# Optimization experiments

Measured on AMD Instinct MI355X. Metric: run time of the kernel, lower is better.

## Reference

```python
import jax, jax.numpy as jnp
import numpy as np

N = 50000
H = 128          # hidden/in/out channels
F = 128          # num_filters
R = 64           # num_rbf
E = 1_600_000    # graph edges
K = 3            # discrete kernel size
RC = 5.0         # cutoff radius


def setup_inputs() -> dict:
    key = jax.random.key(0)
    ks = jax.random.split(key, 16)
    x = jax.random.normal(ks[0], (N, H), dtype=jnp.float32)
    edge_index = jax.random.randint(ks[1], (2, E), 0, N)
    edge_weight = jax.random.uniform(ks[2], (E,), dtype=jnp.float32) * RC
    edge_attr = jax.random.normal(ks[3], (E, R), dtype=jnp.float32)
    # sequential +/-1 neighbor edges (get_seq_neigh): src-dst in {+1,-1}
    i = jnp.arange(N - 1)
    src = jnp.concatenate([i + 1, i])
    dst = jnp.concatenate([i, i + 1])
    disc_edge_index = jnp.stack([src, dst])  # (2, 2*(N-1))

    def xavier(k, shape):
        fan_in, fan_out = shape[1], shape[0]
        lim = jnp.sqrt(6.0 / (fan_in + fan_out)).astype(jnp.float32)
        return jax.random.uniform(k, shape, jnp.float32, -lim, lim)

    return {
        "x": x,
        "edge_weight": edge_weight,
        "edge_attr": edge_attr,
        # filter network: Linear(R,F) -> tanh -> Linear(F,F)
        "fw1": xavier(ks[4], (F, R)), "fb1": jnp.zeros((F,), jnp.float32),
        "fw2": xavier(ks[5], (F, F)), "fb2": jnp.zeros((F,), jnp.float32),
        "lin1_w": xavier(ks[6], (F, H)),                 # no bias
        "lin2_w": xavier(ks[7], (H, F)), "lin2_b": jnp.zeros((H,), jnp.float32),
        "disc_w": xavier(ks[8], (K, F)),                 # DiscConv weight
        "lin_w": xavier(ks[9], (H, H)), "lin_b": jnp.zeros((H,), jnp.float32),
        "edge_index": edge_index,
        "disc_edge_index": disc_edge_index,
    }


def reference(x, edge_weight, edge_attr, fw1, fb1, fw2, fb2,
              lin1_w, lin2_w, lin2_b, disc_w, lin_w, lin_b,
              edge_index, disc_edge_index):
    n = x.shape[0]
    # cosine cutoff envelope
    C = 0.5 * (jnp.cos(edge_weight * (jnp.pi / RC)) + 1.0)
    C = jnp.where(edge_weight < RC, C, 0.0)
    # filter network on expanded distances
    W = jnp.tanh(edge_attr @ fw1.T + fb1) @ fw2.T + fb2
    W = W * C[:, None]                                   # (E, F)
    # lin1 (no bias)
    h = x @ lin1_w.T                                     # (N, F)
    # gather-multiply-scatter message passing
    src, dst = edge_index[0], edge_index[1]
    msg = h[src] * W                                     # (E, F)
    agg = jax.ops.segment_sum(msg, dst, num_segments=n)  # (N, F)
    # discrete sequential convolution (DiscConv)
    dsrc, ddst = disc_edge_index[0], disc_edge_index[1]
    widx = jnp.mod(dsrc - ddst, K)                       # torch weight[-1] == weight[K-1]
    dmsg = disc_w[widx] * h[dsrc]
    disc_out = jax.ops.segment_sum(dmsg, ddst, num_segments=n) + disc_w[0] * h
    h = agg + disc_out
    # lin2 -> tanh -> interaction-block lin
    h = h @ lin2_w.T + lin2_b
    h = jnp.tanh(h)
    return h @ lin_w.T + lin_b
```

## Files before the change

kernel.cpp:

```cpp
#include <hip/hip_runtime.h>
#include <math.h>

#define HD 128
#define FD 128
#define RD 64
#define TE 128
#define RC_CUT 5.0f

typedef _Float16 half8_t __attribute__((ext_vector_type(8)));
typedef float floatx4 __attribute__((ext_vector_type(4)));

__device__ __forceinline__ float fast_tanh(float x) {
    float ex = __expf(2.0f * x);
    return 1.0f - 2.0f / (ex + 1.0f);
}

__global__ __launch_bounds__(256) void lin1_kernel(const float* __restrict__ x,
                                                   const float* __restrict__ w,
                                                   float* __restrict__ h, int n)
{
    __shared__ float sx[16][HD];
    int base = blockIdx.x * 16;
    for (int i = threadIdx.x; i < 16 * HD; i += 256) {
        int r = i >> 7, c = i & 127;
        int row = base + r;
        sx[r][c] = (row < n) ? x[(size_t)row * HD + c] : 0.0f;
    }
    __syncthreads();
    int f = threadIdx.x & 127;
    int half = threadIdx.x >> 7;
    float acc[8];
#pragma unroll
    for (int r = 0; r < 8; ++r) acc[r] = 0.0f;
    const float* wrow = w + (size_t)f * HD;
    for (int k = 0; k < HD; ++k) {
        float wv = wrow[k];
#pragma unroll
        for (int r = 0; r < 8; ++r) acc[r] += sx[half * 8 + r][k] * wv;
    }
#pragma unroll
    for (int r = 0; r < 8; ++r) {
        int row = base + half * 8 + r;
        if (row < n) h[(size_t)row * FD + f] = acc[r];
    }
}

__device__ __forceinline__ half8_t lds_read8(const char* base, int row,
                                             int rowstride, int col) {
    int off = row * rowstride + ((col * 2) ^ ((row & 7) << 4));
    return *(const half8_t*)(base + off);
}

__global__ __launch_bounds__(1024, 8) void edge_kernel(
    const float* __restrict__ edge_weight,
    const float* __restrict__ edge_attr,
    const float* __restrict__ fw1, const float* __restrict__ fb1,
    const float* __restrict__ fw2, const float* __restrict__ fb2,
    const int* __restrict__ eidx,
    const float* __restrict__ h,
    float* agg, int E, int ntiles)
{
    extern __shared__ char smem[];
    char* sT  = smem;
    char* sB1 = smem + 32768;
    char* sB2 = smem + 49152;

    for (int i = threadIdx.x * 8; i < FD * RD; i += blockDim.x * 8) {
        int r = i >> 6, c = i & 63;
        const float4* g = (const float4*)(fw1 + (size_t)r * RD + c);
        float4 v0 = g[0], v1 = g[1];
        half8_t hv;
        hv[0] = (_Float16)v0.x; hv[1] = (_Float16)v0.y;
        hv[2] = (_Float16)v0.z; hv[3] = (_Float16)v0.w;
        hv[4] = (_Float16)v1.x; hv[5] = (_Float16)v1.y;
        hv[6] = (_Float16)v1.z; hv[7] = (_Float16)v1.w;
        *(half8_t*)(sB1 + r * 128 + ((c * 2) ^ ((r & 7) << 4))) = hv;
    }
    for (int i = threadIdx.x * 8; i < FD * FD; i += blockDim.x * 8) {
        int r = i >> 7, c = i & 127;
        const float4* g = (const float4*)(fw2 + (size_t)r * FD + c);
        float4 v0 = g[0], v1 = g[1];
        half8_t hv;
        hv[0] = (_Float16)v0.x; hv[1] = (_Float16)v0.y;
        hv[2] = (_Float16)v0.z; hv[3] = (_Float16)v0.w;
        hv[4] = (_Float16)v1.x; hv[5] = (_Float16)v1.y;
        hv[6] = (_Float16)v1.z; hv[7] = (_Float16)v1.w;
        *(half8_t*)(sB2 + r * 256 + ((c * 2) ^ ((r & 7) << 4))) = hv;
    }
    __syncthreads();

    const int* srcp = eidx;
    const int* dstp = eidx + E;
    int lane = threadIdx.x & 63;
    int wid  = threadIdx.x >> 6;
    int wm = wid >> 2;
    int wn = wid & 3;
    int l15 = lane & 15;
    int l4  = lane >> 4;

    for (int tile = blockIdx.x; tile < ntiles; tile += gridDim.x) {
        int e0 = tile * TE;
        for (int i = threadIdx.x * 8; i < TE * RD; i += blockDim.x * 8) {
            int r = i >> 6, c = i & 63;
            half8_t hv;
            if (e0 + r < E) {
                const float4* g = (const float4*)(edge_attr + (size_t)(e0 + r) * RD + c);
                float4 v0 = g[0], v1 = g[1];
                hv[0] = (_Float16)v0.x; hv[1] = (_Float16)v0.y;
                hv[2] = (_Float16)v0.z; hv[3] = (_Float16)v0.w;
                hv[4] = (_Float16)v1.x; hv[5] = (_Float16)v1.y;
                hv[6] = (_Float16)v1.z; hv[7] = (_Float16)v1.w;
            } else {
                for (int q = 0; q < 8; ++q) hv[q] = (_Float16)0.0f;
            }
            *(half8_t*)(sT + r * 128 + ((c * 2) ^ ((r & 7) << 4))) = hv;
        }
        __syncthreads();

        floatx4 acc[2][2];
#pragma unroll
        for (int mi = 0; mi < 2; ++mi)
#pragma unroll
            for (int ni = 0; ni < 2; ++ni)
                acc[mi][ni] = (floatx4){0.f, 0.f, 0.f, 0.f};
#pragma unroll
        for (int ks = 0; ks < 2; ++ks) {
            int k = ks * 32 + l4 * 8;
            half8_t a[2], b[2];
#pragma unroll
            for (int mi = 0; mi < 2; ++mi)
                a[mi] = lds_read8(sT, wm * 32 + mi * 16 + l15, 128, k);
#pragma unroll
            for (int ni = 0; ni < 2; ++ni)
                b[ni] = lds_read8(sB1, wn * 32 + ni * 16 + l15, 128, k);
#pragma unroll
            for (int mi = 0; mi < 2; ++mi)
#pragma unroll
                for (int ni = 0; ni < 2; ++ni)
                    acc[mi][ni] = __builtin_amdgcn_mfma_f32_16x16x32_f16(
                        a[mi], b[ni], acc[mi][ni], 0, 0, 0);
        }
        __syncthreads();

#pragma unroll
        for (int ni = 0; ni < 2; ++ni) {
            int f = wn * 32 + ni * 16 + l15;
            float bias = fb1[f];
#pragma unroll
            for (int mi = 0; mi < 2; ++mi) {
#pragma unroll
                for (int j = 0; j < 4; ++j) {
                    int e = wm * 32 + mi * 16 + l4 * 4 + j;
                    float t = fast_tanh(acc[mi][ni][j] + bias);
                    *(_Float16*)(sT + e * 256 + ((f * 2) ^ ((e & 7) << 4))) =
                        (_Float16)t;
                }
            }
        }
        __syncthreads();

        floatx4 acc2[2][2];
#pragma unroll
        for (int mi = 0; mi < 2; ++mi)
#pragma unroll
            for (int ni = 0; ni < 2; ++ni)
                acc2[mi][ni] = (floatx4){0.f, 0.f, 0.f, 0.f};
#pragma unroll
        for (int ks = 0; ks < 4; ++ks) {
            int k = ks * 32 + l4 * 8;
            half8_t a[2], b[2];
#pragma unroll
            for (int mi = 0; mi < 2; ++mi)
                a[mi] = lds_read8(sT, wm * 32 + mi * 16 + l15, 256, k);
#pragma unroll
            for (int ni = 0; ni < 2; ++ni)
                b[ni] = lds_read8(sB2, wn * 32 + ni * 16 + l15, 256, k);
#pragma unroll
            for (int mi = 0; mi < 2; ++mi)
#pragma unroll
                for (int ni = 0; ni < 2; ++ni)
                    acc2[mi][ni] = __builtin_amdgcn_mfma_f32_16x16x32_f16(
                        a[mi], b[ni], acc2[mi][ni], 0, 0, 0);
        }
        __syncthreads();

        float bias2[2];
        int gcol[2];
#pragma unroll
        for (int ni = 0; ni < 2; ++ni) {
            gcol[ni] = wn * 32 + ni * 16 + l15;
            bias2[ni] = fb2[gcol[ni]];
        }
#pragma unroll
        for (int mi = 0; mi < 2; ++mi) {
            int ge[4], s4[4], dn4[4];
            float d4[4];
#pragma unroll
            for (int j = 0; j < 4; ++j) {
                int el = wm * 32 + mi * 16 + l4 * 4 + j;
                ge[j] = e0 + el;
                int idx = (ge[j] < E) ? ge[j] : (E - 1);
                s4[j]  = srcp[idx];
                dn4[j] = dstp[idx];
                d4[j]  = edge_weight[idx];
            }
#pragma unroll
            for (int j = 0; j < 4; ++j) {
                if (ge[j] >= E) continue;
                float C = (d4[j] < RC_CUT)
                            ? 0.5f * (__cosf(d4[j] * 0.6283185307179586f) + 1.0f)
                            : 0.0f;
                const float* hrow = h + (size_t)s4[j] * FD;
                float* ar = agg + (size_t)dn4[j] * FD;
#pragma unroll
                for (int ni = 0; ni < 2; ++ni) {
                    int g = gcol[ni];
                    float wv = (acc2[mi][ni][j] + bias2[ni]) * C;
                    atomicAdd(ar + g, wv * hrow[g]);
                }
            }
        }
    }
}

__global__ __launch_bounds__(256) void final_kernel(
    const float* aggin, const float* __restrict__ h,
    const float* __restrict__ disc_w,
    const float* __restrict__ lin2_w, const float* __restrict__ lin2_b,
    const float* __restrict__ lin_w, const float* __restrict__ lin_b,
    float* out, int n)
{
    __shared__ float sg[16][FD];
    __shared__ float sm[16][FD];
    int base = blockIdx.x * 16;
    for (int i = threadIdx.x; i < 16 * FD; i += 256) {
        int r = i >> 7, c = i & 127;
        int row = base + r;
        float v = 0.0f;
        if (row < n) {
            v = aggin[(size_t)row * FD + c] + disc_w[c] * h[(size_t)row * FD + c];
            if (row + 1 < n) v += disc_w[FD + c] * h[(size_t)(row + 1) * FD + c];
            if (row >= 1)    v += disc_w[2 * FD + c] * h[(size_t)(row - 1) * FD + c];
        }
        sg[r][c] = v;
    }
    __syncthreads();
    int f = threadIdx.x & 127;
    int half = threadIdx.x >> 7;
    {
        float acc[8];
        float b = lin2_b[f];
#pragma unroll
        for (int r = 0; r < 8; ++r) acc[r] = b;
        const float* wrow = lin2_w + (size_t)f * FD;
        for (int k = 0; k < FD; ++k) {
            float wv = wrow[k];
#pragma unroll
            for (int r = 0; r < 8; ++r) acc[r] += sg[half * 8 + r][k] * wv;
        }
#pragma unroll
        for (int r = 0; r < 8; ++r) sm[half * 8 + r][f] = fast_tanh(acc[r]);
    }
    __syncthreads();
    {
        float acc[8];
        float b = lin_b[f];
#pragma unroll
        for (int r = 0; r < 8; ++r) acc[r] = b;
        const float* wrow = lin_w + (size_t)f * HD;
        for (int k = 0; k < FD; ++k) {
            float wv = wrow[k];
#pragma unroll
            for (int r = 0; r < 8; ++r) acc[r] += sm[half * 8 + r][k] * wv;
        }
#pragma unroll
        for (int r = 0; r < 8; ++r) {
            int row = base + half * 8 + r;
            if (row < n) out[(size_t)row * HD + f] = acc[r];
        }
    }
}

extern "C" void kernel_launch(void* const* d_in, const int* in_sizes, int n_in,
                              void* d_out, int out_size, void* d_ws, size_t ws_size,
                              hipStream_t stream)
{
    const float* x      = (const float*)d_in[0];
    const float* ew     = (const float*)d_in[1];
    const float* ea     = (const float*)d_in[2];
    const float* fw1    = (const float*)d_in[3];
    const float* fb1    = (const float*)d_in[4];
    const float* fw2    = (const float*)d_in[5];
    const float* fb2    = (const float*)d_in[6];
    const float* lin1_w = (const float*)d_in[7];
    const float* lin2_w = (const float*)d_in[8];
    const float* lin2_b = (const float*)d_in[9];
    const float* disc_w = (const float*)d_in[10];
    const float* lin_w  = (const float*)d_in[11];
    const float* lin_b  = (const float*)d_in[12];
    const int*   eidx   = (const int*)d_in[13];

    int n = in_sizes[0] / HD;
    int E = in_sizes[1];
    float* out = (float*)d_out;
    float* h   = (float*)d_ws;

    hipMemsetAsync(d_out, 0, (size_t)out_size * sizeof(float), stream);

    lin1_kernel<<<(n + 15) / 16, 256, 0, stream>>>(x, lin1_w, h, n);

    int ntiles = (E + TE - 1) / TE;
    size_t smem = 81920;
    hipFuncSetAttribute((const void*)edge_kernel,
                        hipFuncAttributeMaxDynamicSharedMemorySize, (int)smem);
    int nblocks = ntiles < 512 ? ntiles : 512;
    edge_kernel<<<nblocks, 1024, smem, stream>>>(ew, ea, fw1, fb1, fw2, fb2,
                                                 eidx, h, out, E, ntiles);

    final_kernel<<<(n + 15) / 16, 256, 0, stream>>>(out, h, disc_w, lin2_w, lin2_b,
                                                    lin_w, lin_b, out, n);
}
```

Baseline: 876.4 us.

## Bucket edges by destination window and accumulate messages in shared memory

Adds a counting sort of edges into 16-node destination buckets (count, scan, scatter kernels). The edge kernel then pulls buckets from a global work queue, runs the filter MLP on each bucket's edges, and accumulates messages with LDS atomics into a swizzled 16x128 shared buffer. Each bucket writes its rows to agg once, so the global float atomics go away. In exchange it adds three preprocessing passes with global atomics, a serial single-wavefront scan, and indirect gathers of edge_attr, src, dst and weight through perm, which lose coalescing.

Result: slower. 2.399 ms (+173.8%).

```diff
diff --git a/kernel.cpp b/kernel.cpp
--- a/kernel.cpp
+++ b/kernel.cpp
@@ -6,6 +6,8 @@
 #define RD 64
 #define TE 128
 #define RC_CUT 5.0f
+#define WIN 16
+#define WIN_SHIFT 4
 
 typedef _Float16 half8_t __attribute__((ext_vector_type(8)));
 typedef float floatx4 __attribute__((ext_vector_type(4)));
@@ -45,25 +47,72 @@
     }
 }
 
+__global__ __launch_bounds__(256) void count_kernel(const int* __restrict__ dstp,
+                                                    int* cnt, int E)
+{
+    for (int e = blockIdx.x * blockDim.x + threadIdx.x; e < E;
+         e += gridDim.x * blockDim.x)
+        atomicAdd(&cnt[dstp[e] >> WIN_SHIFT], 1);
+}
+
+__global__ void scan_kernel(int* cnt, int* offs, int nbk)
+{
+    int lane = threadIdx.x;
+    int carry = 0;
+    for (int base = 0; base < nbk; base += 64) {
+        int i = base + lane;
+        int v = (i < nbk) ? cnt[i] : 0;
+        int orig = v;
+#pragma unroll
+        for (int d = 1; d < 64; d <<= 1) {
+            int t = __shfl_up(v, d);
+            if (lane >= d) v += t;
+        }
+        if (i < nbk) {
+            int excl = carry + v - orig;
+            offs[i] = excl;
+            cnt[i]  = excl;
+        }
+        carry += __shfl(v, 63);
+    }
+    if (lane == 0) offs[nbk] = carry;
+}
+
+__global__ __launch_bounds__(256) void scatter_kernel(const int* __restrict__ dstp,
+                                                      int* cursor, int* perm, int E)
+{
+    for (int e = blockIdx.x * blockDim.x + threadIdx.x; e < E;
+         e += gridDim.x * blockDim.x) {
+        int p = atomicAdd(&cursor[dstp[e] >> WIN_SHIFT], 1);
+        perm[p] = e;
+    }
+}
+
 __device__ __forceinline__ half8_t lds_read8(const char* base, int row,
                                              int rowstride, int col) {
     int off = row * rowstride + ((col * 2) ^ ((row & 7) << 4));
     return *(const half8_t*)(base + off);
 }
 
-__global__ __launch_bounds__(1024, 8) void edge_kernel(
+__global__ __launch_bounds__(1024, 4) void edge_kernel(
     const float* __restrict__ edge_weight,
     const float* __restrict__ edge_attr,
     const float* __restrict__ fw1, const float* __restrict__ fb1,
     const float* __restrict__ fw2, const float* __restrict__ fb2,
     const int* __restrict__ eidx,
     const float* __restrict__ h,
-    float* agg, int E, int ntiles)
+    const int* __restrict__ perm,
+    const int* __restrict__ offs,
+    int* qctr,
+    float* __restrict__ agg,
+    int E, int n, int nbk)
 {
     extern __shared__ char smem[];
-    char* sT  = smem;
-    char* sB1 = smem + 32768;
-    char* sB2 = smem + 49152;
+    char*  sT   = smem;
+    char*  sB1  = smem + 32768;
+    char*  sB2  = smem + 49152;
+    float* sAgg = (float*)(smem + 81920);
+    __shared__ int sBkt;
 
     for (int i = threadIdx.x * 8; i < FD * RD; i += blockDim.x * 8) {
         int r = i >> 6, c = i & 63;
@@ -87,7 +136,7 @@
         hv[6] = (_Float16)v1.z; hv[7] = (_Float16)v1.w;
         *(half8_t*)(sB2 + r * 256 + ((c * 2) ^ ((r & 7) << 4))) = hv;
     }
-    __syncthreads();
+    for (int i = threadIdx.x; i < WIN * FD; i += blockDim.x) sAgg[i] = 0.0f;
 
     const int* srcp = eidx;
     const int* dstp = eidx + E;
@@ -98,128 +147,157 @@
     int l15 = lane & 15;
     int l4  = lane >> 4;
 
-    for (int tile = blockIdx.x; tile < ntiles; tile += gridDim.x) {
-        int e0 = tile * TE;
-        for (int i = threadIdx.x * 8; i < TE * RD; i += blockDim.x * 8) {
-            int r = i >> 6, c = i & 63;
-            half8_t hv;
-            if (e0 + r < E) {
-                const float4* g = (const float4*)(edge_attr + (size_t)(e0 + r) * RD + c);
-                float4 v0 = g[0], v1 = g[1];
-                hv[0] = (_Float16)v0.x; hv[1] = (_Float16)v0.y;
-                hv[2] = (_Float16)v0.z; hv[3] = (_Float16)v0.w;
-                hv[4] = (_Float16)v1.x; hv[5] = (_Float16)v1.y;
-                hv[6] = (_Float16)v1.z; hv[7] = (_Float16)v1.w;
-            } else {
-                for (int q = 0; q < 8; ++q) hv[q] = (_Float16)0.0f;
+    float bias2[2];
+    float bias1[2];
+    int gcol[2];
+#pragma unroll
+    for (int ni = 0; ni < 2; ++ni) {
+        gcol[ni]  = wn * 32 + ni * 16 + l15;
+        bias2[ni] = fb2[gcol[ni]];
+        bias1[ni] = fb1[gcol[ni]];
+    }
+
+    while (true) {
+        if (threadIdx.x == 0) sBkt = atomicAdd(qctr, 1);
+        __syncthreads();
+        int bkt = sBkt;
+        if (bkt >= nbk) break;
+        int offs0 = offs[bkt];
+        int nE    = offs[bkt + 1] - offs0;
+
+        for (int t0 = 0; t0 < nE; t0 += TE) {
+            {
+                int i = threadIdx.x * 8;
+                int r = i >> 6, c = i & 63;
+                half8_t hv;
+                int ei = t0 + r;
+                if (ei < nE) {
+                    int e = perm[offs0 + ei];
+                    const float4* g = (const float4*)(edge_attr + (size_t)e * RD + c);
+                    float4 v0 = g[0], v1 = g[1];
+                    hv[0] = (_Float16)v0.x; hv[1] = (_Float16)v0.y;
+                    hv[2] = (_Float16)v0.z; hv[3] = (_Float16)v0.w;
+                    hv[4] = (_Float16)v1.x; hv[5] = (_Float16)v1.y;
+                    hv[6] = (_Float16)v1.z; hv[7] = (_Float16)v1.w;
+                } else {
+                    for (int q = 0; q < 8; ++q) hv[q] = (_Float16)0.0f;
+                }
+                *(half8_t*)(sT + r * 128 + ((c * 2) ^ ((r & 7) << 4))) = hv;
             }
-            *(half8_t*)(sT + r * 128 + ((c * 2) ^ ((r & 7) << 4))) = hv;
-        }
-        __syncthreads();
-
-        floatx4 acc[2][2];
-#pragma unroll
-        for (int mi = 0; mi < 2; ++mi)
-#pragma unroll
-            for (int ni = 0; ni < 2; ++ni)
-                acc[mi][ni] = (floatx4){0.f, 0.f, 0.f, 0.f};
-#pragma unroll
-        for (int ks = 0; ks < 2; ++ks) {
-            int k = ks * 32 + l4 * 8;
-            half8_t a[2], b[2];
+            __syncthreads();
+
+            floatx4 acc[2][2];
 #pragma unroll
             for (int mi = 0; mi < 2; ++mi)
-                a[mi] = lds_read8(sT, wm * 32 + mi * 16 + l15, 128, k);
-#pragma unroll
-            for (int ni = 0; ni < 2; ++ni)
-                b[ni] = lds_read8(sB1, wn * 32 + ni * 16 + l15, 128, k);
-#pragma unroll
-            for (int mi = 0; mi < 2; ++mi)
 #pragma unroll
                 for (int ni = 0; ni < 2; ++ni)
-                    acc[mi][ni] = __builtin_amdgcn_mfma_f32_16x16x32_f16(
-                        a[mi], b[ni], acc[mi][ni], 0, 0, 0);
-        }
-        __syncthreads();
-
-#pragma unroll
-        for (int ni = 0; ni < 2; ++ni) {
-            int f = wn * 32 + ni * 16 + l15;
-            float bias = fb1[f];
-#pragma unroll
-            for (int mi = 0; mi < 2; ++mi) {
-#pragma unroll
-                for (int j = 0; j < 4; ++j) {
-                    int e = wm * 32 + mi * 16 + l4 * 4 + j;
-                    float t = fast_tanh(acc[mi][ni][j] + bias);
-                    *(_Float16*)(sT + e * 256 + ((f * 2) ^ ((e & 7) << 4))) =
-                        (_Float16)t;
+                    acc[mi][ni] = (floatx4){0.f, 0.f, 0.f, 0.f};
+#pragma unroll
+            for (int ks = 0; ks < 2; ++ks) {
+                int k = ks * 32 + l4 * 8;
+                half8_t a[2], b[2];
+#pragma unroll
+                for (int mi = 0; mi < 2; ++mi)
+                    a[mi] = lds_read8(sT, wm * 32 + mi * 16 + l15, 128, k);
+#pragma unroll
+                for (int ni = 0; ni < 2; ++ni)
+                    b[ni] = lds_read8(sB1, wn * 32 + ni * 16 + l15, 128, k);
+#pragma unroll
+                for (int mi = 0; mi < 2; ++mi)
+#pragma unroll
+                    for (int ni = 0; ni < 2; ++ni)
+                        acc[mi][ni] = __builtin_amdgcn_mfma_f32_16x16x32_f16(
+                            a[mi], b[ni], acc[mi][ni], 0, 0, 0);
+            }
+            __syncthreads();
+
+#pragma unroll
+            for (int ni = 0; ni < 2; ++ni) {
+                int f = gcol[ni];
+                float bias = bias1[ni];
+#pragma unroll
+                for (int mi = 0; mi < 2; ++mi) {
+#pragma unroll
+                    for (int j = 0; j < 4; ++j) {
+                        int e = wm * 32 + mi * 16 + l4 * 4 + j;
+                        float t = fast_tanh(acc[mi][ni][j] + bias);
+                        *(_Float16*)(sT + e * 256 + ((f * 2) ^ ((e & 7) << 4))) =
+                            (_Float16)t;
+                    }
                 }
             }
-        }
-        __syncthreads();
-
-        floatx4 acc2[2][2];
-#pragma unroll
-        for (int mi = 0; mi < 2; ++mi)
-#pragma unroll
-            for (int ni = 0; ni < 2; ++ni)
-                acc2[mi][ni] = (floatx4){0.f, 0.f, 0.f, 0.f};
-#pragma unroll
-        for (int ks = 0; ks < 4; ++ks) {
-            int k = ks * 32 + l4 * 8;
-            half8_t a[2], b[2];
+            __syncthreads();
+
+            floatx4 acc2[2][2];
 #pragma unroll
             for (int mi = 0; mi < 2; ++mi)
-                a[mi] = lds_read8(sT, wm * 32 + mi * 16 + l15, 256, k);
-#pragma unroll
-            for (int ni = 0; ni < 2; ++ni)
-                b[ni] = lds_read8(sB2, wn * 32 + ni * 16 + l15, 256, k);
-#pragma unroll
-            for (int mi = 0; mi < 2; ++mi)
 #pragma unroll
                 for (int ni = 0; ni < 2; ++ni)
-                    acc2[mi][ni] = __builtin_amdgcn_mfma_f32_16x16x32_f16(
-                        a[mi], b[ni], acc2[mi][ni], 0, 0, 0);
-        }
-        __syncthreads();
-
-        float bias2[2];
-        int gcol[2];
-#pragma unroll
-        for (int ni = 0; ni < 2; ++ni) {
-            gcol[ni] = wn * 32 + ni * 16 + l15;
-            bias2[ni] = fb2[gcol[ni]];
-        }
-#pragma unroll
-        for (int mi = 0; mi < 2; ++mi) {
-            int ge[4], s4[4], dn4[4];
-            float d4[4];
-#pragma unroll
-            for (int j = 0; j < 4; ++j) {
-                int el = wm * 32 + mi * 16 + l4 * 4 + j;
-                ge[j] = e0 + el;
-                int idx = (ge[j] < E) ? ge[j] : (E - 1);
-                s4[j]  = srcp[idx];
-                dn4[j] = dstp[idx];
-                d4[j]  = edge_weight[idx];
+                    acc2[mi][ni] = (floatx4){0.f, 0.f, 0.f, 0.f};
+#pragma unroll
+            for (int ks = 0; ks < 4; ++ks) {
+                int k = ks * 32 + l4 * 8;
+                half8_t a[2], b[2];
+#pragma unroll
+                for (int mi = 0; mi < 2; ++mi)
+                    a[mi] = lds_read8(sT, wm * 32 + mi * 16 + l15, 256, k);
+#pragma unroll
+                for (int ni = 0; ni < 2; ++ni)
+                    b[ni] = lds_read8(sB2, wn * 32 + ni * 16 + l15, 256, k);
+#pragma unroll
+                for (int mi = 0; mi < 2; ++mi)
+#pragma unroll
+                    for (int ni = 0; ni < 2; ++ni)
+                        acc2[mi][ni] = __builtin_amdgcn_mfma_f32_16x16x32_f16(
+                            a[mi], b[ni], acc2[mi][ni], 0, 0, 0);
             }
-#pragma unroll
-            for (int j = 0; j < 4; ++j) {
-                if (ge[j] >= E) continue;
-                float C = (d4[j] < RC_CUT)
-                            ? 0.5f * (__cosf(d4[j] * 0.6283185307179586f) + 1.0f)
-                            : 0.0f;
-                const float* hrow = h + (size_t)s4[j] * FD;
-                float* ar = agg + (size_t)dn4[j] * FD;
-#pragma unroll
-                for (int ni = 0; ni < 2; ++ni) {
-                    int g = gcol[ni];
-                    float wv = (acc2[mi][ni][j] + bias2[ni]) * C;
-                    atomicAdd(ar + g, wv * hrow[g]);
+            __syncthreads();
+
+#pragma unroll
+            for (int mi = 0; mi < 2; ++mi) {
+                int e4[4], s4[4], lr4[4], ok4[4];
+                float d4[4];
+#pragma unroll
+                for (int j = 0; j < 4; ++j) {
+                    int el = wm * 32 + mi * 16 + l4 * 4 + j;
+                    int ei = t0 + el;
+                    ok4[j] = (ei < nE);
+                    e4[j]  = perm[offs0 + (ok4[j] ? ei : 0)];
+                }
+#pragma unroll
+                for (int j = 0; j < 4; ++j) {
+                    s4[j]  = srcp[e4[j]];
+                    lr4[j] = dstp[e4[j]] - (bkt << WIN_SHIFT);
+                    d4[j]  = edge_weight[e4[j]];
+                }
+#pragma unroll
+                for (int j = 0; j < 4; ++j) {
+                    if (!ok4[j]) continue;
+                    float C = (d4[j] < RC_CUT)
+                                ? 0.5f * (__cosf(d4[j] * 0.6283185307179586f) + 1.0f)
+                                : 0.0f;
+                    const float* hrow = h + (size_t)s4[j] * FD;
+                    float* arow = sAgg + lr4[j] * FD;
+                    int rot = (lr4[j] & 7) << 2;
+#pragma unroll
+                    for (int ni = 0; ni < 2; ++ni) {
+                        int g = gcol[ni];
+                        float wv = (acc2[mi][ni][j] + bias2[ni]) * C;
+                        atomicAdd(arow + (g ^ rot), wv * hrow[g]);
+                    }
                 }
             }
         }
+        __syncthreads();
+
+        for (int idx = threadIdx.x; idx < WIN * FD; idx += blockDim.x) {
+            int r = idx >> 7, c = idx & 127;
+            int row = (bkt << WIN_SHIFT) + r;
+            int sa = r * FD + (c ^ ((r & 7) << 2));
+            if (row < n) agg[(size_t)row * FD + c] = sAgg[sa];
+            sAgg[sa] = 0.0f;
+        }
+        __syncthreads();
     }
 }
 
@@ -302,20 +380,33 @@
 
     int n = in_sizes[0] / HD;
     int E = in_sizes[1];
+    int nbk = (n + WIN - 1) / WIN;
     float* out = (float*)d_out;
-    float* h   = (float*)d_ws;
+
+    char* base = (char*)d_ws;
+    float* h    = (float*)base;
+    int*   perm = (int*)(base + (size_t)n * FD * 4);
+    int*   cnt  = (int*)(base + (size_t)n * FD * 4 + (size_t)E * 4);
+    int*   offs = cnt + nbk;
+    int*   qctr = offs + nbk + 1;
+
+    const int* dstp = eidx + E;
 
     hipMemsetAsync(d_out, 0, (size_t)out_size * sizeof(float), stream);
+    hipMemsetAsync(cnt, 0, (size_t)(2 * nbk + 2) * sizeof(int), stream);
+
+    count_kernel<<<2048, 256, 0, stream>>>(dstp, cnt, E);
+    scan_kernel<<<1, 64, 0, stream>>>(cnt, offs, nbk);
+    scatter_kernel<<<2048, 256, 0, stream>>>(dstp, cnt, perm, E);
 
     lin1_kernel<<<(n + 15) / 16, 256, 0, stream>>>(x, lin1_w, h, n);
 
-    int ntiles = (E + TE - 1) / TE;
-    size_t smem = 81920;
+    size_t smem = 90112;
     hipFuncSetAttribute((const void*)edge_kernel,
                         hipFuncAttributeMaxDynamicSharedMemorySize, (int)smem);
-    int nblocks = ntiles < 512 ? ntiles : 512;
-    edge_kernel<<<nblocks, 1024, smem, stream>>>(ew, ea, fw1, fb1, fw2, fb2,
-                                                 eidx, h, out, E, ntiles);
+    edge_kernel<<<256, 1024, smem, stream>>>(ew, ea, fw1, fb1, fw2, fb2,
+                                             eidx, h, perm, offs, qctr,
+                                             out, E, n, nbk);
 
     final_kernel<<<(n + 15) / 16, 256, 0, stream>>>(out, h, disc_w, lin2_w, lin2_b,
                                                     lin_w, lin_b, out, n);
```

## Bucket edges by destination window and aggregate in shared memory

Applied to the files above, without the earlier changes.

Adds a counting sort of edges by 16-node destination windows (count, scan and scatter kernels). The filter-network GEMM kernel now writes the per-edge fp16 filter W into the sorted position. A new aggregation kernel then gathers h, multiplies, and accumulates each window in LDS with shared-memory atomics instead of global float atomics. This removes global atomic contention, but adds a large fp16 W round trip through memory plus several preprocessing launches. The old atomic kernel remains as a fallback when the workspace is too small or n exceeds 16-bit indices.

After: 1.916 ms. 119% more time.

```diff
diff --git a/kernel.cpp b/kernel.cpp
--- a/kernel.cpp
+++ b/kernel.cpp
@@ -6,6 +6,8 @@
 #define RD 64
 #define TE 128
 #define RC_CUT 5.0f
+#define WIN 16
+#define WIN_SHIFT 4
 
 typedef _Float16 half8_t __attribute__((ext_vector_type(8)));
 typedef float floatx4 __attribute__((ext_vector_type(4)));
@@ -45,20 +47,64 @@
     }
 }
 
+__global__ __launch_bounds__(256) void count_kernel(const int* __restrict__ dstp,
+                                                    int* cnt, int E)
+{
+    for (int e = blockIdx.x * blockDim.x + threadIdx.x; e < E;
+         e += gridDim.x * blockDim.x)
+        atomicAdd(&cnt[dstp[e] >> WIN_SHIFT], 1);
+}
+
+__global__ void scan_kernel(int* cnt, int* offs, int nbk)
+{
+    int lane = threadIdx.x;
+    int carry = 0;
+    for (int base = 0; base < nbk; base += 64) {
+        int i = base + lane;
+        int v = (i < nbk) ? cnt[i] : 0;
+        int orig = v;
+#pragma unroll
+        for (int d = 1; d < 64; d <<= 1) {
+            int t = __shfl_up(v, d);
+            if (lane >= d) v += t;
+        }
+        if (i < nbk) {
+            int excl = carry + v - orig;
+            offs[i] = excl;
+            cnt[i]  = excl;
+        }
+        carry += __shfl(v, 63);
+    }
+    if (lane == 0) offs[nbk] = carry;
+}
+
+__global__ __launch_bounds__(256) void scatter_kernel(
+    const int* __restrict__ srcp, const int* __restrict__ dstp,
+    int* cursor, int* __restrict__ inv, unsigned int* __restrict__ meta, int E)
+{
+    for (int e = blockIdx.x * blockDim.x + threadIdx.x; e < E;
+         e += gridDim.x * blockDim.x) {
+        int d = dstp[e];
+        int p = atomicAdd(&cursor[d >> WIN_SHIFT], 1);
+        inv[e] = p;
+        meta[p] = (unsigned int)srcp[e] | ((unsigned int)(d & (WIN - 1)) << 16);
+    }
+}
+
 __device__ __forceinline__ half8_t lds_read8(const char* base, int row,
                                              int rowstride, int col) {
     int off = row * rowstride + ((col * 2) ^ ((row & 7) << 4));
     return *(const half8_t*)(base + off);
 }
 
-__global__ __launch_bounds__(1024, 8) void edge_kernel(
+__global__ __launch_bounds__(1024, 8) void edge_gemm_kernel(
     const float* __restrict__ edge_weight,
     const float* __restrict__ edge_attr,
     const float* __restrict__ fw1, const float* __restrict__ fb1,
     const float* __restrict__ fw2, const float* __restrict__ fb2,
-    const int* __restrict__ eidx,
-    const float* __restrict__ h,
-    float* agg, int E, int ntiles)
+    const int* __restrict__ inv,
+    _Float16* __restrict__ Wp,
+    int E, int ntiles)
 {
     extern __shared__ char smem[];
     char* sT  = smem;
@@ -89,14 +135,21 @@
     }
     __syncthreads();
 
-    const int* srcp = eidx;
-    const int* dstp = eidx + E;
     int lane = threadIdx.x & 63;
     int wid  = threadIdx.x >> 6;
     int wm = wid >> 2;
     int wn = wid & 3;
     int l15 = lane & 15;
     int l4  = lane >> 4;
+
+    float bias1[2], bias2[2];
+    int gcol[2];
+#pragma unroll
+    for (int ni = 0; ni < 2; ++ni) {
+        gcol[ni]  = wn * 32 + ni * 16 + l15;
+        bias1[ni] = fb1[gcol[ni]];
+        bias2[ni] = fb2[gcol[ni]];
+    }
 
     for (int tile = blockIdx.x; tile < ntiles; tile += gridDim.x) {
         int e0 = tile * TE;
@@ -144,6 +197,206 @@
 
 #pragma unroll
         for (int ni = 0; ni < 2; ++ni) {
+            int f = gcol[ni];
+            float bias = bias1[ni];
+#pragma unroll
+            for (int mi = 0; mi < 2; ++mi) {
+#pragma unroll
+                for (int j = 0; j < 4; ++j) {
+                    int e = wm * 32 + mi * 16 + l4 * 4 + j;
+                    float t = fast_tanh(acc[mi][ni][j] + bias);
+                    *(_Float16*)(sT + e * 256 + ((f * 2) ^ ((e & 7) << 4))) =
+                        (_Float16)t;
+                }
+            }
+        }
+        __syncthreads();
+
+        floatx4 acc2[2][2];
+#pragma unroll
+        for (int mi = 0; mi < 2; ++mi)
+#pragma unroll
+            for (int ni = 0; ni < 2; ++ni)
+                acc2[mi][ni] = (floatx4){0.f, 0.f, 0.f, 0.f};
+#pragma unroll
+        for (int ks = 0; ks < 4; ++ks) {
+            int k = ks * 32 + l4 * 8;
+            half8_t a[2], b[2];
+#pragma unroll
+            for (int mi = 0; mi < 2; ++mi)
+                a[mi] = lds_read8(sT, wm * 32 + mi * 16 + l15, 256, k);
+#pragma unroll
+            for (int ni = 0; ni < 2; ++ni)
+                b[ni] = lds_read8(sB2, wn * 32 + ni * 16 + l15, 256, k);
+#pragma unroll
+            for (int mi = 0; mi < 2; ++mi)
+#pragma unroll
+                for (int ni = 0; ni < 2; ++ni)
+                    acc2[mi][ni] = __builtin_amdgcn_mfma_f32_16x16x32_f16(
+                        a[mi], b[ni], acc2[mi][ni], 0, 0, 0);
+        }
+        __syncthreads();
+
+#pragma unroll
+        for (int mi = 0; mi < 2; ++mi) {
+            int ge[4], pv[4];
+            float d4[4];
+#pragma unroll
+            for (int j = 0; j < 4; ++j) {
+                int el = wm * 32 + mi * 16 + l4 * 4 + j;
+                ge[j] = e0 + el;
+                int idx = (ge[j] < E) ? ge[j] : (E - 1);
+                d4[j] = edge_weight[idx];
+                pv[j] = inv[idx];
+            }
+#pragma unroll
+            for (int j = 0; j < 4; ++j) {
+                if (ge[j] >= E) continue;
+                float C = (d4[j] < RC_CUT)
+                            ? 0.5f * (__cosf(d4[j] * 0.6283185307179586f) + 1.0f)
+                            : 0.0f;
+                _Float16* wr = Wp + (size_t)pv[j] * FD;
+#pragma unroll
+                for (int ni = 0; ni < 2; ++ni)
+                    wr[gcol[ni]] = (_Float16)((acc2[mi][ni][j] + bias2[ni]) * C);
+            }
+        }
+    }
+}
+
+__global__ __launch_bounds__(256) void agg_kernel(
+    const _Float16* __restrict__ Wp,
+    const unsigned int* __restrict__ meta,
+    const int* __restrict__ offs,
+    const float* __restrict__ h,
+    float* __restrict__ agg, int n)
+{
+    __shared__ float sAgg[WIN * FD];
+    for (int i = threadIdx.x; i < WIN * FD; i += 256) sAgg[i] = 0.0f;
+    __syncthreads();
+
+    int bkt = blockIdx.x;
+    int o0 = offs[bkt];
+    int nE = offs[bkt + 1] - o0;
+    int lane = threadIdx.x & 63;
+    int wv = threadIdx.x >> 6;
+
+    for (int i = wv; i < nE; i += 4) {
+        int p = o0 + i;
+        unsigned int m = meta[p];
+        int src = m & 0xFFFF;
+        int lr = m >> 16;
+        const _Float16* wr = Wp + (size_t)p * FD;
+        float w0 = (float)wr[lane];
+        float w1 = (float)wr[64 + lane];
+        const float* hr = h + (size_t)src * FD;
+        float h0 = hr[lane];
+        float h1 = hr[64 + lane];
+        atomicAdd(&sAgg[lr * FD + lane], w0 * h0);
+        atomicAdd(&sAgg[lr * FD + 64 + lane], w1 * h1);
+    }
+    __syncthreads();
+
+    int r0 = bkt << WIN_SHIFT;
+    for (int i = threadIdx.x; i < WIN * FD; i += 256) {
+        int r = i >> 7;
+        if (r0 + r < n) agg[(size_t)(r0 + r) * FD + (i & 127)] = sAgg[i];
+    }
+}
+
+__global__ __launch_bounds__(1024, 8) void edge_kernel_atomic(
+    const float* __restrict__ edge_weight,
+    const float* __restrict__ edge_attr,
+    const float* __restrict__ fw1, const float* __restrict__ fb1,
+    const float* __restrict__ fw2, const float* __restrict__ fb2,
+    const int* __restrict__ eidx,
+    const float* __restrict__ h,
+    float* agg, int E, int ntiles)
+{
+    extern __shared__ char smem[];
+    char* sT  = smem;
+    char* sB1 = smem + 32768;
+    char* sB2 = smem + 49152;
+
+    for (int i = threadIdx.x * 8; i < FD * RD; i += blockDim.x * 8) {
+        int r = i >> 6, c = i & 63;
+        const float4* g = (const float4*)(fw1 + (size_t)r * RD + c);
+        float4 v0 = g[0], v1 = g[1];
+        half8_t hv;
+        hv[0] = (_Float16)v0.x; hv[1] = (_Float16)v0.y;
+        hv[2] = (_Float16)v0.z; hv[3] = (_Float16)v0.w;
+        hv[4] = (_Float16)v1.x; hv[5] = (_Float16)v1.y;
+        hv[6] = (_Float16)v1.z; hv[7] = (_Float16)v1.w;
+        *(half8_t*)(sB1 + r * 128 + ((c * 2) ^ ((r & 7) << 4))) = hv;
+    }
+    for (int i = threadIdx.x * 8; i < FD * FD; i += blockDim.x * 8) {
+        int r = i >> 7, c = i & 127;
+        const float4* g = (const float4*)(fw2 + (size_t)r * FD + c);
+        float4 v0 = g[0], v1 = g[1];
+        half8_t hv;
+        hv[0] = (_Float16)v0.x; hv[1] = (_Float16)v0.y;
+        hv[2] = (_Float16)v0.z; hv[3] = (_Float16)v0.w;
+        hv[4] = (_Float16)v1.x; hv[5] = (_Float16)v1.y;
+        hv[6] = (_Float16)v1.z; hv[7] = (_Float16)v1.w;
+        *(half8_t*)(sB2 + r * 256 + ((c * 2) ^ ((r & 7) << 4))) = hv;
+    }
+    __syncthreads();
+
+    const int* srcp = eidx;
+    const int* dstp = eidx + E;
+    int lane = threadIdx.x & 63;
+    int wid  = threadIdx.x >> 6;
+    int wm = wid >> 2;
+    int wn = wid & 3;
+    int l15 = lane & 15;
+    int l4  = lane >> 4;
+
+    for (int tile = blockIdx.x; tile < ntiles; tile += gridDim.x) {
+        int e0 = tile * TE;
+        for (int i = threadIdx.x * 8; i < TE * RD; i += blockDim.x * 8) {
+            int r = i >> 6, c = i & 63;
+            half8_t hv;
+            if (e0 + r < E) {
+                const float4* g = (const float4*)(edge_attr + (size_t)(e0 + r) * RD + c);
+                float4 v0 = g[0], v1 = g[1];
+                hv[0] = (_Float16)v0.x; hv[1] = (_Float16)v0.y;
+                hv[2] = (_Float16)v0.z; hv[3] = (_Float16)v0.w;
+                hv[4] = (_Float16)v1.x; hv[5] = (_Float16)v1.y;
+                hv[6] = (_Float16)v1.z; hv[7] = (_Float16)v1.w;
+            } else {
+                for (int q = 0; q < 8; ++q) hv[q] = (_Float16)0.0f;
+            }
+            *(half8_t*)(sT + r * 128 + ((c * 2) ^ ((r & 7) << 4))) = hv;
+        }
+        __syncthreads();
+
+        floatx4 acc[2][2];
+#pragma unroll
+        for (int mi = 0; mi < 2; ++mi)
+#pragma unroll
+            for (int ni = 0; ni < 2; ++ni)
+                acc[mi][ni] = (floatx4){0.f, 0.f, 0.f, 0.f};
+#pragma unroll
+        for (int ks = 0; ks < 2; ++ks) {
+            int k = ks * 32 + l4 * 8;
+            half8_t a[2], b[2];
+#pragma unroll
+            for (int mi = 0; mi < 2; ++mi)
+                a[mi] = lds_read8(sT, wm * 32 + mi * 16 + l15, 128, k);
+#pragma unroll
+            for (int ni = 0; ni < 2; ++ni)
+                b[ni] = lds_read8(sB1, wn * 32 + ni * 16 + l15, 128, k);
+#pragma unroll
+            for (int mi = 0; mi < 2; ++mi)
+#pragma unroll
+                for (int ni = 0; ni < 2; ++ni)
+                    acc[mi][ni] = __builtin_amdgcn_mfma_f32_16x16x32_f16(
+                        a[mi], b[ni], acc[mi][ni], 0, 0, 0);
+        }
+        __syncthreads();
+
+#pragma unroll
+        for (int ni = 0; ni < 2; ++ni) {
             int f = wn * 32 + ni * 16 + l15;
             float bias = fb1[f];
 #pragma unroll
@@ -302,20 +555,50 @@
 
     int n = in_sizes[0] / HD;
     int E = in_sizes[1];
+    int nbk = (n + WIN - 1) / WIN;
+    int ntiles = (E + TE - 1) / TE;
     float* out = (float*)d_out;
-    float* h   = (float*)d_ws;
+
+    const int* srcp = eidx;
+    const int* dstp = eidx + E;
+
+    char* base = (char*)d_ws;
+    float*     h    = (float*)base;
+    size_t off_h    = (size_t)n * FD * 4;
+    _Float16*  Wp   = (_Float16*)(base + off_h);
+    size_t off_w    = off_h + (size_t)E * FD * 2;
+    int*       inv  = (int*)(base + off_w);
+    size_t off_i    = off_w + (size_t)E * 4;
+    unsigned int* meta = (unsigned int*)(base + off_i);
+    size_t off_m    = off_i + (size_t)E * 4;
+    int*       cnt  = (int*)(base + off_m);
+    int*       offs = cnt + nbk;
+    size_t need     = off_m + (size_t)(2 * nbk + 8) * 4;
 
     hipMemsetAsync(d_out, 0, (size_t)out_size * sizeof(float), stream);
-
     lin1_kernel<<<(n + 15) / 16, 256, 0, stream>>>(x, lin1_w, h, n);
 
-    int ntiles = (E + TE - 1) / TE;
     size_t smem = 81920;
-    hipFuncSetAttribute((const void*)edge_kernel,
-                        hipFuncAttributeMaxDynamicSharedMemorySize, (int)smem);
-    int nblocks = ntiles < 512 ? ntiles : 512;
-    edge_kernel<<<nblocks, 1024, smem, stream>>>(ew, ea, fw1, fb1, fw2, fb2,
-                                                 eidx, h, out, E, ntiles);
+    if (ws_size >= need && n <= 65535) {
+        hipMemsetAsync(cnt, 0, (size_t)(2 * nbk + 2) * sizeof(int), stream);
+        count_kernel<<<2048, 256, 0, stream>>>(dstp, cnt, E);
+        scan_kernel<<<1, 64, 0, stream>>>(cnt, offs, nbk);
+        scatter_kernel<<<2048, 256, 0, stream>>>(srcp, dstp, cnt, inv, meta, E);
+
+        hipFuncSetAttribute((const void*)edge_gemm_kernel,
+                            hipFuncAttributeMaxDynamicSharedMemorySize, (int)smem);
+        int nblocks = ntiles < 512 ? ntiles : 512;
+        edge_gemm_kernel<<<nblocks, 1024, smem, stream>>>(ew, ea, fw1, fb1, fw2, fb2,
+                                                          inv, Wp, E, ntiles);
+
+        agg_kernel<<<nbk, 256, 0, stream>>>(Wp, meta, offs, h, out, n);
+    } else {
+        hipFuncSetAttribute((const void*)edge_kernel_atomic,
+                            hipFuncAttributeMaxDynamicSharedMemorySize, (int)smem);
+        int nblocks = ntiles < 512 ? ntiles : 512;
+        edge_kernel_atomic<<<nblocks, 1024, smem, stream>>>(ew, ea, fw1, fb1, fw2, fb2,
+                                                            eidx, h, out, E, ntiles);
+    }
 
     final_kernel<<<(n + 15) / 16, 256, 0, stream>>>(out, h, disc_w, lin2_w, lin2_b,
                                                     lin_w, lin_b, out, n);
```
